# Kernel optimization log

Hardware: AMD Instinct MI355X
Metric: run time of the kernel (lower is better)

The kernel has to match this reference:

```python
import jax, jax.numpy as jnp
import numpy as np

B, IN, CTRL, M, V, OUT = 2048, 64, 512, 1024, 64, 64


def setup_inputs() -> dict:
    key = jax.random.key(0)
    ks = jax.random.split(key, 20)
    s = 0.05  # small param scale for numerical stability

    def rn(k, shape, scale):
        return jax.random.normal(k, shape, dtype=jnp.float32) * scale

    return {
        # forward args
        "x": rn(ks[0], (B, IN), 1.0),
        "h_prev": rn(ks[1], (B, CTRL), 0.1),
        "c_prev": rn(ks[2], (B, CTRL), 0.1),
        "read_weights_prev": jax.nn.softmax(rn(ks[3], (B, M), 1.0), axis=1),
        # parameters
        "memory": rn(ks[4], (M, V), 1.0),
        "W_ih": rn(ks[5], (4 * CTRL, IN + V), s),
        "b_ih": rn(ks[6], (4 * CTRL,), s),
        "W_hh": rn(ks[7], (4 * CTRL, CTRL), s),
        "b_hh": rn(ks[8], (4 * CTRL,), s),
        "W_read": rn(ks[9], (M, CTRL), s),
        "b_read": rn(ks[10], (M,), s),
        "W_write": rn(ks[11], (M, CTRL), s),
        "b_write": rn(ks[12], (M,), s),
        "W_erase": rn(ks[13], (V, CTRL), s),
        "b_erase": rn(ks[14], (V,), s),
        "W_add": rn(ks[15], (V, CTRL), s),
        "b_add": rn(ks[16], (V,), s),
        "W_out": rn(ks[17], (OUT, CTRL + V), s),
        "b_out": rn(ks[18], (OUT,), s),
    }


def reference(x, h_prev, c_prev, read_weights_prev, memory,
              W_ih, b_ih, W_hh, b_hh,
              W_read, b_read, W_write, b_write,
              W_erase, b_erase, W_add, b_add,
              W_out, b_out):
    # read with previous weights on pre-write memory: [B,M] @ [M,V] -> [B,V]
    read_prev = read_weights_prev @ memory
    inp = jnp.concatenate([x, read_prev], axis=1)  # [B, IN+V]

    # LSTMCell (PyTorch gate order: i, f, g, o)
    gates = inp @ W_ih.T + b_ih + h_prev @ W_hh.T + b_hh  # [B, 4*CTRL]
    i, f, g, o = jnp.split(gates, 4, axis=1)
    i = jax.nn.sigmoid(i)
    f = jax.nn.sigmoid(f)
    g = jnp.tanh(g)
    o = jax.nn.sigmoid(o)
    c = f * c_prev + i * g
    h = o * jnp.tanh(c)

    # addressing + erase/add vectors
    read_w = jax.nn.softmax(h @ W_read.T + b_read, axis=1)    # [B,M]
    write_w = jax.nn.softmax(h @ W_write.T + b_write, axis=1)  # [B,M]
    erase = jax.nn.sigmoid(h @ W_erase.T + b_erase)            # [B,V]
    add = jnp.tanh(h @ W_add.T + b_add)                        # [B,V]

    # outer-product erase/add memory update: [B,M,V]
    w = write_w[:, :, None]
    mem_new = memory[None, :, :] * (1.0 - w * erase[:, None, :]) + w * add[:, None, :]

    # read with new weights on post-write memory
    read_new = jnp.einsum('bm,bmv->bv', read_w, mem_new)

    out = jnp.concatenate([h, read_new], axis=1) @ W_out.T + b_out  # [B,OUT]
    return out
```

## Files before the change

### kernel.cpp

```cpp
#include <hip/hip_runtime.h>
#include <hip/hip_bf16.h>


typedef unsigned short u16;
typedef __attribute__((ext_vector_type(8))) short bf16x8;
typedef __attribute__((ext_vector_type(4))) float f32x4;

#define MFMA_BF16(a, b, c) __builtin_amdgcn_mfma_f32_16x16x32_bf16((a), (b), (c), 0, 0, 0)
#define LDW 136

__device__ __forceinline__ void dma16(const void* g, void* l) {
    __builtin_amdgcn_global_load_lds(
        (const __attribute__((address_space(1))) unsigned int*)g,
        (__attribute__((address_space(3))) unsigned int*)l, 16, 0, 0);
}

__device__ __forceinline__ u16 f2bf(float f) {
    union { float f; unsigned int u; } a; a.f = f;
    return (u16)((a.u + 0x7FFFu + ((a.u >> 16) & 1u)) >> 16);
}

__device__ __forceinline__ void pack_store4(float a0, float a1, float a2, float a3, u16* d) {
    union { __hip_bfloat162 h[2]; uint2 u; } cv;
    cv.h[0] = __float22bfloat162_rn(make_float2(a0, a1));
    cv.h[1] = __float22bfloat162_rn(make_float2(a2, a3));
    *(uint2*)d = cv.u;
}

__device__ __forceinline__ void cvt4(const float* __restrict__ s, u16* __restrict__ d) {
    float4 v = *(const float4*)s;
    pack_store4(v.x, v.y, v.z, v.w, d);
}

__device__ __forceinline__ uint4 cvt8u(const float* __restrict__ s) {
    float4 v0 = *(const float4*)(s);
    float4 v1 = *(const float4*)(s + 4);
    union { __hip_bfloat162 h[4]; uint4 u; } r;
    r.h[0] = __float22bfloat162_rn(make_float2(v0.x, v0.y));
    r.h[1] = __float22bfloat162_rn(make_float2(v0.z, v0.w));
    r.h[2] = __float22bfloat162_rn(make_float2(v1.x, v1.y));
    r.h[3] = __float22bfloat162_rn(make_float2(v1.z, v1.w));
    return r.u;
}

__device__ __forceinline__ uint4 cvt8u_sum4(const float* __restrict__ p, int off) {
    float4 a0 = *(const float4*)(p + off);
    float4 a1 = *(const float4*)(p + 131072 + off);
    float4 a2 = *(const float4*)(p + 262144 + off);
    float4 a3 = *(const float4*)(p + 393216 + off);
    float4 b0 = *(const float4*)(p + off + 4);
    float4 b1 = *(const float4*)(p + 131072 + off + 4);
    float4 b2 = *(const float4*)(p + 262144 + off + 4);
    float4 b3 = *(const float4*)(p + 393216 + off + 4);
    float4 s0{a0.x + a1.x + a2.x + a3.x, a0.y + a1.y + a2.y + a3.y,
              a0.z + a1.z + a2.z + a3.z, a0.w + a1.w + a2.w + a3.w};
    float4 s1{b0.x + b1.x + b2.x + b3.x, b0.y + b1.y + b2.y + b3.y,
              b0.z + b1.z + b2.z + b3.z, b0.w + b1.w + b2.w + b3.w};
    union { __hip_bfloat162 h[4]; uint4 u; } r;
    r.h[0] = __float22bfloat162_rn(make_float2(s0.x, s0.y));
    r.h[1] = __float22bfloat162_rn(make_float2(s0.z, s0.w));
    r.h[2] = __float22bfloat162_rn(make_float2(s1.x, s1.y));
    r.h[3] = __float22bfloat162_rn(make_float2(s1.z, s1.w));
    return r.u;
}

__device__ __forceinline__ void bfu4_to_f8(uint4 u, float* f) {
    f[0] = __uint_as_float(u.x << 16); f[1] = __uint_as_float(u.x & 0xffff0000u);
    f[2] = __uint_as_float(u.y << 16); f[3] = __uint_as_float(u.y & 0xffff0000u);
    f[4] = __uint_as_float(u.z << 16); f[5] = __uint_as_float(u.z & 0xffff0000u);
    f[6] = __uint_as_float(u.w << 16); f[7] = __uint_as_float(u.w & 0xffff0000u);
}

__device__ __forceinline__ uint4 pack8(const float* v) {
    union { __hip_bfloat162 h[4]; uint4 u; } r;
#pragma unroll
    for (int j = 0; j < 4; ++j) r.h[j] = __float22bfloat162_rn(make_float2(v[2 * j], v[2 * j + 1]));
    return r.u;
}

__device__ __forceinline__ float sigf(float x) { return 1.f / (1.f + __expf(-x)); }
__device__ __forceinline__ float fast_tanh(float x) { return 1.f - 2.f / (__expf(2.f * x) + 1.f); }

__global__ __launch_bounds__(256) void k_pre(
    const float* __restrict__ x, const float* __restrict__ h_prev, const float* __restrict__ rwp,
    const float* __restrict__ memory, const float* __restrict__ W_ih, const float* __restrict__ W_hh,
    const float* __restrict__ W_read, const float* __restrict__ W_write, const float* __restrict__ W_erase,
    const float* __restrict__ W_add, const float* __restrict__ W_out,
    u16* x_t, u16* ht_t, u16* wcat_t, u16* Wcat2_t, u16* Wo_rn, u16* memt, float* rp)
{
    __shared__ u16 As[64 * LDW];
    __shared__ u16 Bs[64 * LDW];
    const int tid = threadIdx.x;

    if (blockIdx.x < 128) {
        const int mb = blockIdx.x & 31, ks = blockIdx.x >> 5;
        const int w = tid >> 6, lane = tid & 63;
        const int lrow = lane & 15, lq = lane >> 4;
        const int m0 = mb * 64, k0 = ks * 256;
        const int m_loc = tid >> 1, v0 = (tid & 1) * 32;
        f32x4 acc[4] = {};
        for (int kt = 0; kt < 2; ++kt) {
#pragma unroll
            for (int i = 0; i < 4; ++i) {
                int idx = i * 256 + tid, r = idx >> 4, c = (idx & 15) * 8;
                *(uint4*)(&As[r * LDW + c]) = cvt8u(rwp + (m0 + r) * 1024 + k0 + kt * 128 + c);
            }
#pragma unroll
            for (int j = 0; j < 8; ++j) {
                float4 q = *(const float4*)(memory + (k0 + kt * 128 + m_loc) * 64 + v0 + 4 * j);
                Bs[(v0 + 4 * j + 0) * LDW + m_loc] = f2bf(q.x);
                Bs[(v0 + 4 * j + 1) * LDW + m_loc] = f2bf(q.y);
                Bs[(v0 + 4 * j + 2) * LDW + m_loc] = f2bf(q.z);
                Bs[(v0 + 4 * j + 3) * LDW + m_loc] = f2bf(q.w);
            }
            __syncthreads();
#pragma unroll
            for (int kk = 0; kk < 128; kk += 32) {
                bf16x8 a  = *(const bf16x8*)(&As[(16 * w + lrow) * LDW + kk + 8 * lq]);
                bf16x8 b0 = *(const bf16x8*)(&Bs[(lrow) * LDW + kk + 8 * lq]);
                bf16x8 b1 = *(const bf16x8*)(&Bs[(16 + lrow) * LDW + kk + 8 * lq]);
                bf16x8 b2 = *(const bf16x8*)(&Bs[(32 + lrow) * LDW + kk + 8 * lq]);
                bf16x8 b3 = *(const bf16x8*)(&Bs[(48 + lrow) * LDW + kk + 8 * lq]);
                acc[0] = MFMA_BF16(a, b0, acc[0]);
                acc[1] = MFMA_BF16(a, b1, acc[1]);
                acc[2] = MFMA_BF16(a, b2, acc[2]);
                acc[3] = MFMA_BF16(a, b3, acc[3]);
            }
            __syncthreads();
        }
        float* rps = rp + ks * 131072;
#pragma unroll
        for (int nj = 0; nj < 4; ++nj)
#pragma unroll
            for (int r = 0; r < 4; ++r) {
                int row = m0 + 16 * w + 4 * lq + r, col = 16 * nj + lrow;
                rps[row * 64 + col] = acc[nj][r];
            }
        return;
    }

    int t = (blockIdx.x - 128) * 256 + tid;
    if (t < 32768) {
        int r = t >> 4, c = (t & 15) * 4;
        cvt4(x + r * 64 + c, x_t + ((r >> 7) * 8 + (c >> 3)) * 1024 + (r & 127) * 8 + (c & 7));
        return;
    }
    t -= 32768;
    if (t < 262144) {
        int r = t >> 7, c = (t & 127) * 4;
        cvt4(h_prev + r * 512 + c, ht_t + ((r >> 7) * 64 + (c >> 3)) * 1024 + (r & 127) * 8 + (c & 7));
        return;
    }
    t -= 262144;
    if (t < 65536) {
        int r = t >> 5, c = (t & 31) * 4;
        int g = r >> 9, j = r & 511;
        int bn = j >> 4, row64 = (g << 4) + (j & 15);
        int cd = (c < 64) ? c + 64 : c - 64;
        cvt4(W_ih + r * 128 + c, wcat_t + (bn * 5) * 8192 + (cd >> 3) * 512 + row64 * 8 + (cd & 7));
        return;
    }
    t -= 65536;
    if (t < 262144) {
        int r = t >> 7, c = (t & 127) * 4;
        int g = r >> 9, j = r & 511;
        int bn = j >> 4, row64 = (g << 4) + (j & 15);
        int cd = 128 + c;
        cvt4(W_hh + r * 512 + c, wcat_t + (bn * 5 + (cd >> 7)) * 8192 + ((cd >> 3) & 15) * 512 + row64 * 8 + (cd & 7));
        return;
    }
    t -= 262144;
    if (t < 131072) {
        int r = t >> 7, c = (t & 127) * 4;
        cvt4(W_read + t * 4, Wcat2_t + ((r >> 6) * 4 + (c >> 7)) * 8192 + ((c >> 3) & 15) * 512 + (r & 63) * 8 + (c & 7));
        return;
    }
    t -= 131072;
    if (t < 131072) {
        int r = t >> 7, c = (t & 127) * 4;
        cvt4(W_write + t * 4, Wcat2_t + ((16 + (r >> 6)) * 4 + (c >> 7)) * 8192 + ((c >> 3) & 15) * 512 + (r & 63) * 8 + (c & 7));
        return;
    }
    t -= 131072;
    if (t < 8192) {
        int r = t >> 7, c = (t & 127) * 4;
        cvt4(W_erase + t * 4, Wcat2_t + (32 * 4 + (c >> 7)) * 8192 + ((c >> 3) & 15) * 512 + r * 8 + (c & 7));
        return;
    }
    t -= 8192;
    if (t < 8192) {
        int r = t >> 7, c = (t & 127) * 4;
        cvt4(W_add + t * 4, Wcat2_t + (33 * 4 + (c >> 7)) * 8192 + ((c >> 3) & 15) * 512 + r * 8 + (c & 7));
        return;
    }
    t -= 8192;
    if (t < 9216) {
        int r = t / 144, c = (t % 144) * 4;
        if (c < 512)
            cvt4(W_out + r * 576 + c, Wcat2_t + (34 * 4 + (c >> 7)) * 8192 + ((c >> 3) & 15) * 512 + r * 8 + (c & 7));
        else
            cvt4(W_out + r * 576 + c, Wo_rn + r * 64 + (c - 512));
        return;
    }
    t -= 9216;
    if (t < 16384) {
        int v = t >> 8, m = (t & 255) * 4;
        pack_store4(memory[m * 64 + v], memory[(m + 1) * 64 + v],
                    memory[(m + 2) * 64 + v], memory[(m + 3) * 64 + v], memt + v * 1024 + m);
    }
}

__global__ __launch_bounds__(256) void k_gates(const u16* __restrict__ x_t, const u16* __restrict__ ht_t,
                                               const float* __restrict__ rp, const u16* __restrict__ wcat_t,
                                               const float* __restrict__ b_ih, const float* __restrict__ b_hh,
                                               const float* __restrict__ c_prev, u16* __restrict__ hrn_t)
{
    __shared__ u16 As[16384];
    __shared__ u16 Bs[8192];
    const int tid = threadIdx.x, w = tid >> 6, lane = tid & 63;
    const int lrow = lane & 15, lq = lane >> 4;
    const int mt = blockIdx.x, bn = blockIdx.y;
    const int m0 = mt * 128;
    f32x4 acc[2][4] = {};
    for (int kt = 0; kt < 5; ++kt) {
        if (kt == 0) {
#pragma unroll
            for (int i = 0; i < 4; ++i) {
                int cp = i * 256 + tid;
                int oct = cp >> 7, row = cp & 127;
                *(uint4*)(&As[cp * 8]) = cvt8u_sum4(rp, (m0 + row) * 64 + oct * 8);
            }
#pragma unroll
            for (int i = 0; i < 4; ++i) {
                int cp = i * 256 + tid;
                dma16(x_t + mt * 8192 + cp * 8, &As[(1024 + (i * 256 + w * 64)) * 8]);
            }
        } else {
#pragma unroll
            for (int i = 0; i < 8; ++i) {
                int cp = i * 256 + tid;
                dma16(ht_t + mt * 65536 + (kt - 1) * 16384 + cp * 8, &As[(i * 256 + w * 64) * 8]);
            }
        }
#pragma unroll
        for (int i = 0; i < 4; ++i) {
            int cp = i * 256 + tid;
            dma16(wcat_t + (bn * 5 + kt) * 8192 + cp * 8, &Bs[(i * 256 + w * 64) * 8]);
        }
        __syncthreads();
#pragma unroll
        for (int kk = 0; kk < 128; kk += 32) {
            const int ob = (kk >> 3) + lq;
            bf16x8 a0 = *(const bf16x8*)(&As[ob * 1024 + (32 * w + lrow) * 8]);
            bf16x8 a1 = *(const bf16x8*)(&As[ob * 1024 + (32 * w + 16 + lrow) * 8]);
            bf16x8 b0 = *(const bf16x8*)(&Bs[ob * 512 + (lrow) * 8]);
            bf16x8 b1 = *(const bf16x8*)(&Bs[ob * 512 + (16 + lrow) * 8]);
            bf16x8 b2 = *(const bf16x8*)(&Bs[ob * 512 + (32 + lrow) * 8]);
            bf16x8 b3 = *(const bf16x8*)(&Bs[ob * 512 + (48 + lrow) * 8]);
            acc[0][0] = MFMA_BF16(a0, b0, acc[0][0]);
            acc[0][1] = MFMA_BF16(a0, b1, acc[0][1]);
            acc[0][2] = MFMA_BF16(a0, b2, acc[0][2]);
            acc[0][3] = MFMA_BF16(a0, b3, acc[0][3]);
            acc[1][0] = MFMA_BF16(a1, b0, acc[1][0]);
            acc[1][1] = MFMA_BF16(a1, b1, acc[1][1]);
            acc[1][2] = MFMA_BF16(a1, b2, acc[1][2]);
            acc[1][3] = MFMA_BF16(a1, b3, acc[1][3]);
        }
        __syncthreads();
    }
    const int j = bn * 16 + lrow;
    const float bI = b_ih[j] + b_hh[j];
    const float bF = b_ih[512 + j] + b_hh[512 + j];
    const float bG = b_ih[1024 + j] + b_hh[1024 + j];
    const float bO = b_ih[1536 + j] + b_hh[1536 + j];
#pragma unroll
    for (int mi = 0; mi < 2; ++mi)
#pragma unroll
        for (int r = 0; r < 4; ++r) {
            int row = m0 + 32 * w + 16 * mi + 4 * lq + r;
            float ig = sigf(acc[mi][0][r] + bI);
            float fg = sigf(acc[mi][1][r] + bF);
            float gg = fast_tanh(acc[mi][2][r] + bG);
            float og = sigf(acc[mi][3][r] + bO);
            float c = fg * c_prev[row * 512 + j] + ig * gg;
            hrn_t[(row >> 7) * 65536 + (j >> 3) * 1024 + (row & 127) * 8 + (j & 7)] =
                f2bf(og * fast_tanh(c));
        }
}

__global__ __launch_bounds__(256) void k_heads(const u16* __restrict__ hrn_t, const u16* __restrict__ Wcat2_t,
                                               const float* __restrict__ b_read, const float* __restrict__ b_write,
                                               const float* __restrict__ b_erase, const float* __restrict__ b_add,
                                               const float* __restrict__ b_out,
                                               u16* __restrict__ pre_r, u16* __restrict__ pre_w,
                                               float* __restrict__ erase, float* __restrict__ add,
                                               float* __restrict__ out)
{
    __shared__ u16 As[16384];
    __shared__ u16 Bs[8192];
    const int tid = threadIdx.x, w = tid >> 6, lane = tid & 63;
    const int lrow = lane & 15, lq = lane >> 4;
    const int mt = blockIdx.x, bn = blockIdx.y;
    const int m0 = mt * 128;
    f32x4 acc[2][4] = {};
    for (int kt = 0; kt < 4; ++kt) {
#pragma unroll
        for (int i = 0; i < 8; ++i) {
            int cp = i * 256 + tid;
            dma16(hrn_t + mt * 65536 + kt * 16384 + cp * 8, &As[(i * 256 + w * 64) * 8]);
        }
#pragma unroll
        for (int i = 0; i < 4; ++i) {
            int cp = i * 256 + tid;
            dma16(Wcat2_t + (bn * 4 + kt) * 8192 + cp * 8, &Bs[(i * 256 + w * 64) * 8]);
        }
        __syncthreads();
#pragma unroll
        for (int kk = 0; kk < 128; kk += 32) {
            const int ob = (kk >> 3) + lq;
            bf16x8 a0 = *(const bf16x8*)(&As[ob * 1024 + (32 * w + lrow) * 8]);
            bf16x8 a1 = *(const bf16x8*)(&As[ob * 1024 + (32 * w + 16 + lrow) * 8]);
            bf16x8 b0 = *(const bf16x8*)(&Bs[ob * 512 + (lrow) * 8]);
            bf16x8 b1 = *(const bf16x8*)(&Bs[ob * 512 + (16 + lrow) * 8]);
            bf16x8 b2 = *(const bf16x8*)(&Bs[ob * 512 + (32 + lrow) * 8]);
            bf16x8 b3 = *(const bf16x8*)(&Bs[ob * 512 + (48 + lrow) * 8]);
            acc[0][0] = MFMA_BF16(a0, b0, acc[0][0]);
            acc[0][1] = MFMA_BF16(a0, b1, acc[0][1]);
            acc[0][2] = MFMA_BF16(a0, b2, acc[0][2]);
            acc[0][3] = MFMA_BF16(a0, b3, acc[0][3]);
            acc[1][0] = MFMA_BF16(a1, b0, acc[1][0]);
            acc[1][1] = MFMA_BF16(a1, b1, acc[1][1]);
            acc[1][2] = MFMA_BF16(a1, b2, acc[1][2]);
            acc[1][3] = MFMA_BF16(a1, b3, acc[1][3]);
        }
        __syncthreads();
    }
#pragma unroll
    for (int mi = 0; mi < 2; ++mi)
#pragma unroll
        for (int nj = 0; nj < 4; ++nj)
#pragma unroll
            for (int r = 0; r < 4; ++r) {
                int row = m0 + 32 * w + 16 * mi + 4 * lq + r;
                int col = bn * 64 + 16 * nj + lrow;
                float v = acc[mi][nj][r];
                if (bn < 16)       pre_r[row * 1024 + col] = f2bf(v + b_read[col]);
                else if (bn < 32)  pre_w[row * 1024 + (col - 1024)] = f2bf(v + b_write[col - 1024]);
                else if (bn == 32) erase[row * 64 + (col - 2048)] = sigf(v + b_erase[col - 2048]);
                else if (bn == 33) add[row * 64 + (col - 2112)] = fast_tanh(v + b_add[col - 2112]);
                else               out[row * 64 + (col - 2176)] = v + b_out[col - 2176];
            }
}

#define SLDW 520

__global__ __launch_bounds__(256) void k_tail(const u16* __restrict__ pre_r, const u16* __restrict__ pre_w,
                                              const u16* __restrict__ memt, const u16* __restrict__ Wo_rn,
                                              const float* __restrict__ erase, const float* __restrict__ add,
                                              float* __restrict__ out)
{
    __shared__ u16 rwS[16 * SLDW];
    __shared__ u16 rw2S[16 * SLDW];
    __shared__ u16 BsP[64 * LDW];
    __shared__ u16 Ps[16 * 72];
    __shared__ float s_sh[16];
    const int tid = threadIdx.x, w = tid >> 6, lane = tid & 63;
    const int lrow = lane & 15, lq = lane >> 4;
    const int mb = blockIdx.x >> 1, kh = blockIdx.x & 1;
    const int m0 = mb * 16, k0 = kh * 512;

    {
        const int row = tid >> 4, c16 = tid & 15;
        const int row_g = m0 + row;
        const u16* prp = pre_r + row_g * 1024;
        const u16* pwp = pre_w + row_g * 1024;
        float vr[64], vw[64];
#pragma unroll
        for (int q = 0; q < 8; ++q) {
            bfu4_to_f8(*(const uint4*)(prp + q * 128 + c16 * 8), vr + 8 * q);
            bfu4_to_f8(*(const uint4*)(pwp + q * 128 + c16 * 8), vw + 8 * q);
        }
        float mr = vr[0], mw = vw[0];
#pragma unroll
        for (int i = 1; i < 64; ++i) { mr = fmaxf(mr, vr[i]); mw = fmaxf(mw, vw[i]); }
#pragma unroll
        for (int o = 1; o < 16; o <<= 1) {
            mr = fmaxf(mr, __shfl_xor(mr, o, 64));
            mw = fmaxf(mw, __shfl_xor(mw, o, 64));
        }
        float sr = 0.f, sw = 0.f;
#pragma unroll
        for (int i = 0; i < 64; ++i) {
            vr[i] = __expf(vr[i] - mr); sr += vr[i];
            vw[i] = __expf(vw[i] - mw); sw += vw[i];
        }
#pragma unroll
        for (int o = 1; o < 16; o <<= 1) {
            sr += __shfl_xor(sr, o, 64);
            sw += __shfl_xor(sw, o, 64);
        }
        const float isr = 1.f / sr, isw = 1.f / sw;
        float ss = 0.f;
#pragma unroll
        for (int q = 0; q < 8; ++q) {
            float a8[8], r8[8];
#pragma unroll
            for (int i = 0; i < 8; ++i) {
                float a = vr[8 * q + i] * isr;
                float r2 = a * (vw[8 * q + i] * isw);
                a8[i] = a; r8[i] = r2;
                ss += r2;
            }
            if ((q >> 2) == kh) {
                int cb = (q - 4 * kh) * 128 + c16 * 8;
                *(uint4*)(&rwS[row * SLDW + cb])  = pack8(a8);
                *(uint4*)(&rw2S[row * SLDW + cb]) = pack8(r8);
            }
        }
#pragma unroll
        for (int o = 1; o < 16; o <<= 1) ss += __shfl_xor(ss, o, 64);
        if (c16 == 0) s_sh[row] = ss;
    }
    __syncthreads();

    f32x4 acc1 = {}, acc2 = {};
    for (int kt = 0; kt < 4; ++kt) {
#pragma unroll
        for (int i = 0; i < 4; ++i) {
            int idx = i * 256 + tid, r = idx >> 4, c = (idx & 15) * 8;
            *(uint4*)(&BsP[r * LDW + c]) = *(const uint4*)(memt + r * 1024 + k0 + kt * 128 + c);
        }
        __syncthreads();
#pragma unroll
        for (int kk = 0; kk < 128; kk += 32) {
            bf16x8 a1 = *(const bf16x8*)(&rwS[lrow * SLDW + kt * 128 + kk + 8 * lq]);
            bf16x8 a2 = *(const bf16x8*)(&rw2S[lrow * SLDW + kt * 128 + kk + 8 * lq]);
            bf16x8 b  = *(const bf16x8*)(&BsP[(16 * w + lrow) * LDW + kk + 8 * lq]);
            acc1 = MFMA_BF16(a1, b, acc1);
            acc2 = MFMA_BF16(a2, b, acc2);
        }
        __syncthreads();
    }

#pragma unroll
    for (int r = 0; r < 4; ++r) {
        int row_l = 4 * lq + r, col = 16 * w + lrow;
        int row_g = m0 + row_l;
        float p = acc1[r] - erase[row_g * 64 + col] * acc2[r];
        if (kh == 0) p += add[row_g * 64 + col] * s_sh[row_l];
        Ps[row_l * 72 + col] = f2bf(p);
    }
#pragma unroll
    for (int i = 0; i < 2; ++i) {
        int idx = i * 256 + tid, r = idx >> 3, c = (idx & 7) * 8;
        *(uint4*)(&BsP[r * LDW + c]) = *(const uint4*)(Wo_rn + r * 64 + c);
    }
    __syncthreads();

    f32x4 acc3 = {};
#pragma unroll
    for (int kk = 0; kk < 64; kk += 32) {
        bf16x8 a = *(const bf16x8*)(&Ps[lrow * 72 + kk + 8 * lq]);
        bf16x8 b = *(const bf16x8*)(&BsP[(16 * w + lrow) * LDW + kk + 8 * lq]);
        acc3 = MFMA_BF16(a, b, acc3);
    }
#pragma unroll
    for (int r = 0; r < 4; ++r) {
        int row_g = m0 + 4 * lq + r, col = 16 * w + lrow;
        atomicAdd(&out[row_g * 64 + col], acc3[r]);
    }
}

extern "C" void kernel_launch(void* const* d_in, const int* in_sizes, int n_in,
                              void* d_out, int out_size, void* d_ws, size_t ws_size,
                              hipStream_t stream)
{
    const float* x        = (const float*)d_in[0];
    const float* h_prev   = (const float*)d_in[1];
    const float* c_prev   = (const float*)d_in[2];
    const float* rwp      = (const float*)d_in[3];
    const float* memory   = (const float*)d_in[4];
    const float* W_ih     = (const float*)d_in[5];
    const float* b_ih     = (const float*)d_in[6];
    const float* W_hh     = (const float*)d_in[7];
    const float* b_hh     = (const float*)d_in[8];
    const float* W_read   = (const float*)d_in[9];
    const float* b_read   = (const float*)d_in[10];
    const float* W_write  = (const float*)d_in[11];
    const float* b_write  = (const float*)d_in[12];
    const float* W_erase  = (const float*)d_in[13];
    const float* b_erase  = (const float*)d_in[14];
    const float* W_add    = (const float*)d_in[15];
    const float* b_add    = (const float*)d_in[16];
    const float* W_out    = (const float*)d_in[17];
    const float* b_out    = (const float*)d_in[18];
    float* out = (float*)d_out;

    char* wsp = (char*)d_ws;
    u16*   x_t     = (u16*)(wsp + 0);
    u16*   ht_t    = (u16*)(wsp + 262144);
    u16*   wcat_t  = (u16*)(wsp + 2359296);
    u16*   memt    = (u16*)(wsp + 4980736);
    u16*   Wcat2_t = (u16*)(wsp + 5111808);
    u16*   Wo_rn   = (u16*)(wsp + 7405568);
    float* rp      = (float*)(wsp + 7413760);
    u16*   hrn_t   = (u16*)(wsp + 9510912);
    u16*   pre_r   = (u16*)(wsp + 11608064);
    u16*   pre_w   = (u16*)(wsp + 15802368);
    float* erase   = (float*)(wsp + 19996672);
    float* add     = (float*)(wsp + 20520960);

    k_pre<<<3748, 256, 0, stream>>>(x, h_prev, rwp, memory, W_ih, W_hh, W_read, W_write,
                                    W_erase, W_add, W_out,
                                    x_t, ht_t, wcat_t, Wcat2_t, Wo_rn, memt, rp);
    k_gates<<<dim3(16, 32), 256, 0, stream>>>(x_t, ht_t, rp, wcat_t, b_ih, b_hh, c_prev, hrn_t);
    k_heads<<<dim3(16, 35), 256, 0, stream>>>(hrn_t, Wcat2_t, b_read, b_write, b_erase, b_add, b_out,
                                              pre_r, pre_w, erase, add, out);
    k_tail<<<256, 256, 0, stream>>>(pre_r, pre_w, memt, Wo_rn, erase, add, out);
}
```

Baseline: 158.1 us.

## Double-buffer LDS tiles in gates and heads GEMMs to overlap loads with MFMA

Splits the K-tiles of the k_gates and k_heads GEMM loops into half-size (64-wide) chunks held in two LDS buffers. The next chunk is prefetched by async global-to-LDS DMA while MFMAs run on the current one, and partial vmcnt waits replace full __syncthreads. The aim is to hide global load latency that was previously exposed on every K step. In exchange there are twice as many barrier iterations, and correctness depends on the hand-counted vmcnt value matching the number of outstanding DMA ops.

New measurement: 157.5 us. About the same (-0.4%).

```diff
diff --git a/kernel.cpp b/kernel.cpp
--- a/kernel.cpp
+++ b/kernel.cpp
@@ -81,6 +81,23 @@
 __device__ __forceinline__ float sigf(float x) { return 1.f / (1.f + __expf(-x)); }
 __device__ __forceinline__ float fast_tanh(float x) { return 1.f - 2.f / (__expf(2.f * x) + 1.f); }
 
+#define PIPE_BAR_PRE_CNT()  do {                                              \
+    asm volatile("s_waitcnt vmcnt(6) lgkmcnt(0)" ::: "memory");               \
+    __builtin_amdgcn_s_barrier();                                             \
+    __builtin_amdgcn_sched_barrier(0);                                        \
+} while (0)
+#define PIPE_BAR_PRE_ZERO() do {                                              \
+    asm volatile("s_waitcnt vmcnt(0) lgkmcnt(0)" ::: "memory");               \
+    __builtin_amdgcn_s_barrier();                                             \
+    __builtin_amdgcn_sched_barrier(0);                                        \
+} while (0)
+#define PIPE_BAR_POST() do {                                                  \
+    __builtin_amdgcn_sched_barrier(0);                                        \
+    asm volatile("s_waitcnt lgkmcnt(0)" ::: "memory");                        \
+    __builtin_amdgcn_s_barrier();                                             \
+    __builtin_amdgcn_sched_barrier(0);                                        \
+} while (0)
+
 __global__ __launch_bounds__(256) void k_pre(
     const float* __restrict__ x, const float* __restrict__ h_prev, const float* __restrict__ rwp,
     const float* __restrict__ memory, const float* __restrict__ W_ih, const float* __restrict__ W_hh,
@@ -215,48 +232,56 @@
                                                const float* __restrict__ b_ih, const float* __restrict__ b_hh,
                                                const float* __restrict__ c_prev, u16* __restrict__ hrn_t)
 {
-    __shared__ u16 As[16384];
-    __shared__ u16 Bs[8192];
+    __shared__ u16 As[2][8192];
+    __shared__ u16 Bs[2][4096];
     const int tid = threadIdx.x, w = tid >> 6, lane = tid & 63;
     const int lrow = lane & 15, lq = lane >> 4;
     const int mt = blockIdx.x, bn = blockIdx.y;
     const int m0 = mt * 128;
     f32x4 acc[2][4] = {};
-    for (int kt = 0; kt < 5; ++kt) {
-        if (kt == 0) {
+
+#pragma unroll
+    for (int i = 0; i < 4; ++i) {
+        int cp = i * 256 + tid;
+        *(uint4*)(&As[0][cp * 8]) = cvt8u_sum4(rp, (m0 + (cp & 127)) * 64 + (cp >> 7) * 8);
+    }
+#pragma unroll
+    for (int i = 0; i < 2; ++i) {
+        int cp = i * 256 + tid;
+        dma16(wcat_t + (bn * 5) * 8192 + cp * 8, &Bs[0][(i * 256 + w * 64) * 8]);
+    }
+
+#pragma unroll
+    for (int t = 0; t < 10; ++t) {
+        if (t < 9) {
+            const int tn = t + 1, b = tn & 1;
+            const u16* asrc = (tn == 1) ? (x_t + mt * 8192)
+                                        : (ht_t + mt * 65536 + (tn - 2) * 8192);
 #pragma unroll
             for (int i = 0; i < 4; ++i) {
                 int cp = i * 256 + tid;
-                int oct = cp >> 7, row = cp & 127;
-                *(uint4*)(&As[cp * 8]) = cvt8u_sum4(rp, (m0 + row) * 64 + oct * 8);
-            }
-#pragma unroll
-            for (int i = 0; i < 4; ++i) {
+                dma16(asrc + cp * 8, &As[b][(i * 256 + w * 64) * 8]);
+            }
+#pragma unroll
+            for (int i = 0; i < 2; ++i) {
                 int cp = i * 256 + tid;
-                dma16(x_t + mt * 8192 + cp * 8, &As[(1024 + (i * 256 + w * 64)) * 8]);
-            }
+                dma16(wcat_t + (bn * 5 + (tn >> 1)) * 8192 + (tn & 1) * 4096 + cp * 8,
+                      &Bs[b][(i * 256 + w * 64) * 8]);
+            }
+            PIPE_BAR_PRE_CNT();
         } else {
-#pragma unroll
-            for (int i = 0; i < 8; ++i) {
-                int cp = i * 256 + tid;
-                dma16(ht_t + mt * 65536 + (kt - 1) * 16384 + cp * 8, &As[(i * 256 + w * 64) * 8]);
-            }
-        }
-#pragma unroll
-        for (int i = 0; i < 4; ++i) {
-            int cp = i * 256 + tid;
-            dma16(wcat_t + (bn * 5 + kt) * 8192 + cp * 8, &Bs[(i * 256 + w * 64) * 8]);
-        }
-        __syncthreads();
-#pragma unroll
-        for (int kk = 0; kk < 128; kk += 32) {
+            PIPE_BAR_PRE_ZERO();
+        }
+        const int b = t & 1;
+#pragma unroll
+        for (int kk = 0; kk < 64; kk += 32) {
             const int ob = (kk >> 3) + lq;
-            bf16x8 a0 = *(const bf16x8*)(&As[ob * 1024 + (32 * w + lrow) * 8]);
-            bf16x8 a1 = *(const bf16x8*)(&As[ob * 1024 + (32 * w + 16 + lrow) * 8]);
-            bf16x8 b0 = *(const bf16x8*)(&Bs[ob * 512 + (lrow) * 8]);
-            bf16x8 b1 = *(const bf16x8*)(&Bs[ob * 512 + (16 + lrow) * 8]);
-            bf16x8 b2 = *(const bf16x8*)(&Bs[ob * 512 + (32 + lrow) * 8]);
-            bf16x8 b3 = *(const bf16x8*)(&Bs[ob * 512 + (48 + lrow) * 8]);
+            bf16x8 a0 = *(const bf16x8*)(&As[b][ob * 1024 + (32 * w + lrow) * 8]);
+            bf16x8 a1 = *(const bf16x8*)(&As[b][ob * 1024 + (32 * w + 16 + lrow) * 8]);
+            bf16x8 b0 = *(const bf16x8*)(&Bs[b][ob * 512 + (lrow) * 8]);
+            bf16x8 b1 = *(const bf16x8*)(&Bs[b][ob * 512 + (16 + lrow) * 8]);
+            bf16x8 b2 = *(const bf16x8*)(&Bs[b][ob * 512 + (32 + lrow) * 8]);
+            bf16x8 b3 = *(const bf16x8*)(&Bs[b][ob * 512 + (48 + lrow) * 8]);
             acc[0][0] = MFMA_BF16(a0, b0, acc[0][0]);
             acc[0][1] = MFMA_BF16(a0, b1, acc[0][1]);
             acc[0][2] = MFMA_BF16(a0, b2, acc[0][2]);
@@ -266,8 +291,9 @@
             acc[1][2] = MFMA_BF16(a1, b2, acc[1][2]);
             acc[1][3] = MFMA_BF16(a1, b3, acc[1][3]);
         }
-        __syncthreads();
-    }
+        PIPE_BAR_POST();
+    }
+
     const int j = bn * 16 + lrow;
     const float bI = b_ih[j] + b_hh[j];
     const float bF = b_ih[512 + j] + b_hh[512 + j];
@@ -296,34 +322,54 @@
                                                float* __restrict__ erase, float* __restrict__ add,
                                                float* __restrict__ out)
 {
-    __shared__ u16 As[16384];
-    __shared__ u16 Bs[8192];
+    __shared__ u16 As[2][8192];
+    __shared__ u16 Bs[2][4096];
     const int tid = threadIdx.x, w = tid >> 6, lane = tid & 63;
     const int lrow = lane & 15, lq = lane >> 4;
     const int mt = blockIdx.x, bn = blockIdx.y;
     const int m0 = mt * 128;
     f32x4 acc[2][4] = {};
-    for (int kt = 0; kt < 4; ++kt) {
-#pragma unroll
-        for (int i = 0; i < 8; ++i) {
-            int cp = i * 256 + tid;
-            dma16(hrn_t + mt * 65536 + kt * 16384 + cp * 8, &As[(i * 256 + w * 64) * 8]);
-        }
-#pragma unroll
-        for (int i = 0; i < 4; ++i) {
-            int cp = i * 256 + tid;
-            dma16(Wcat2_t + (bn * 4 + kt) * 8192 + cp * 8, &Bs[(i * 256 + w * 64) * 8]);
-        }
-        __syncthreads();
-#pragma unroll
-        for (int kk = 0; kk < 128; kk += 32) {
+
+#pragma unroll
+    for (int i = 0; i < 4; ++i) {
+        int cp = i * 256 + tid;
+        dma16(hrn_t + mt * 65536 + cp * 8, &As[0][(i * 256 + w * 64) * 8]);
+    }
+#pragma unroll
+    for (int i = 0; i < 2; ++i) {
+        int cp = i * 256 + tid;
+        dma16(Wcat2_t + (bn * 4) * 8192 + cp * 8, &Bs[0][(i * 256 + w * 64) * 8]);
+    }
+
+#pragma unroll
+    for (int t = 0; t < 8; ++t) {
+        if (t < 7) {
+            const int tn = t + 1, b = tn & 1;
+#pragma unroll
+            for (int i = 0; i < 4; ++i) {
+                int cp = i * 256 + tid;
+                dma16(hrn_t + mt * 65536 + tn * 8192 + cp * 8, &As[b][(i * 256 + w * 64) * 8]);
+            }
+#pragma unroll
+            for (int i = 0; i < 2; ++i) {
+                int cp = i * 256 + tid;
+                dma16(Wcat2_t + (bn * 4 + (tn >> 1)) * 8192 + (tn & 1) * 4096 + cp * 8,
+                      &Bs[b][(i * 256 + w * 64) * 8]);
+            }
+            PIPE_BAR_PRE_CNT();
+        } else {
+            PIPE_BAR_PRE_ZERO();
+        }
+        const int b = t & 1;
+#pragma unroll
+        for (int kk = 0; kk < 64; kk += 32) {
             const int ob = (kk >> 3) + lq;
-            bf16x8 a0 = *(const bf16x8*)(&As[ob * 1024 + (32 * w + lrow) * 8]);
-            bf16x8 a1 = *(const bf16x8*)(&As[ob * 1024 + (32 * w + 16 + lrow) * 8]);
-            bf16x8 b0 = *(const bf16x8*)(&Bs[ob * 512 + (lrow) * 8]);
-            bf16x8 b1 = *(const bf16x8*)(&Bs[ob * 512 + (16 + lrow) * 8]);
-            bf16x8 b2 = *(const bf16x8*)(&Bs[ob * 512 + (32 + lrow) * 8]);
-            bf16x8 b3 = *(const bf16x8*)(&Bs[ob * 512 + (48 + lrow) * 8]);
+            bf16x8 a0 = *(const bf16x8*)(&As[b][ob * 1024 + (32 * w + lrow) * 8]);
+            bf16x8 a1 = *(const bf16x8*)(&As[b][ob * 1024 + (32 * w + 16 + lrow) * 8]);
+            bf16x8 b0 = *(const bf16x8*)(&Bs[b][ob * 512 + (lrow) * 8]);
+            bf16x8 b1 = *(const bf16x8*)(&Bs[b][ob * 512 + (16 + lrow) * 8]);
+            bf16x8 b2 = *(const bf16x8*)(&Bs[b][ob * 512 + (32 + lrow) * 8]);
+            bf16x8 b3 = *(const bf16x8*)(&Bs[b][ob * 512 + (48 + lrow) * 8]);
             acc[0][0] = MFMA_BF16(a0, b0, acc[0][0]);
             acc[0][1] = MFMA_BF16(a0, b1, acc[0][1]);
             acc[0][2] = MFMA_BF16(a0, b2, acc[0][2]);
@@ -333,8 +379,9 @@
             acc[1][2] = MFMA_BF16(a1, b2, acc[1][2]);
             acc[1][3] = MFMA_BF16(a1, b3, acc[1][3]);
         }
-        __syncthreads();
-    }
+        PIPE_BAR_POST();
+    }
+
 #pragma unroll
     for (int mi = 0; mi < 2; ++mi)
 #pragma unroll
```
